# Optimization experiments

Hardware: AMD Instinct MI355X
Metric: run time of the kernel (lower is better)

## Reference

```python
import jax, jax.numpy as jnp
import numpy as np

MAX_FPS = 30.0
NUM_HEADS = 8


def _rope(x, times):
    # x: [B, H, T, D] with D even; interleaved rotary (even/odd pairs)
    B, H, T, D = x.shape
    inv_freq = 1.0 / (10000.0 ** (jnp.arange(0, D, 2, dtype=jnp.float32) / D))  # [D/2]
    pos = jnp.round(times * MAX_FPS)                       # [B, T]
    freqs = pos[:, :, None] * inv_freq[None, None, :]      # [B, T, D/2]
    cos = jnp.cos(freqs)[:, None, :, :]                    # [B, 1, T, D/2]
    sin = jnp.sin(freqs)[:, None, :, :]
    xp = x.reshape(B, H, T, D // 2, 2)
    x0, x1 = xp[..., 0], xp[..., 1]                        # even-index, odd-index elems
    r0 = x0 * cos - x1 * sin
    r1 = x0 * sin + x1 * cos
    return jnp.stack([r0, r1], axis=-1).reshape(B, H, T, D)


def setup_inputs() -> dict:
    key = jax.random.key(0)
    k1, k2, k3, k4, k5 = jax.random.split(key, 5)
    B, N, C = 4, 2048, 512
    x = jax.random.normal(k1, (B, N, C), dtype=jnp.float32)
    mask = jnp.zeros((B, N), dtype=jnp.float32)  # additive mask, 0 = attend
    # times in seconds; rounded to frame indices inside RoPE
    times = jax.random.uniform(k2, (B, N), dtype=jnp.float32) * (N / MAX_FPS)
    bound_qkv = float(np.sqrt(6.0 / (C + 3 * C)))
    Wqkv = jax.random.uniform(k3, (3 * C, C), minval=-bound_qkv, maxval=bound_qkv, dtype=jnp.float32)
    bound_p = float(np.sqrt(6.0 / (C + C)))
    Wproj = jax.random.uniform(k4, (C, C), minval=-bound_p, maxval=bound_p, dtype=jnp.float32)
    bproj = jnp.zeros((C,), dtype=jnp.float32)
    return {"x": x, "mask": mask, "times": times, "Wqkv": Wqkv,
            "Wproj": Wproj, "bproj": bproj, "num_cls_token": 0}


def reference(x, mask, times, Wqkv, Wproj, bproj, num_cls_token):
    B, N, C = x.shape
    H = NUM_HEADS
    Dh = C // H
    qkv = (x @ Wqkv.T).reshape(B, N, 3, H, Dh).transpose(2, 0, 3, 1, 4)  # [3,B,H,N,Dh]
    q, k, v = qkv[0], qkv[1], qkv[2]
    if num_cls_token > 0:
        c_q, q = q[:, :, :num_cls_token], q[:, :, num_cls_token:]
        c_k, k = k[:, :, :num_cls_token], k[:, :, num_cls_token:]
        t = times
        q = _rope(q, t)
        k = _rope(k, t)
        q = jnp.concatenate([c_q, q], axis=2)
        k = jnp.concatenate([c_k, k], axis=2)
    else:
        q = _rope(q, times)
        k = _rope(k, times)
    scale = 1.0 / jnp.sqrt(jnp.float32(Dh))
    scores = jnp.einsum('bhqd,bhkd->bhqk', q, k) * scale + mask[:, None, None, :]
    attn = jax.nn.softmax(scores, axis=-1)
    out = jnp.einsum('bhqk,bhkd->bhqd', attn, v)           # [B,H,N,Dh]
    out = out.transpose(0, 2, 1, 3).reshape(B, N, C)
    return out @ Wproj.T + bproj
```

## Files before the change

### kernel.cpp

```cpp
#include <hip/hip_runtime.h>
#include <math.h>

#define BB 4
#define NN 2048
#define CC 512
#define HH 8
#define DH 64
#define MM (BB*NN)
#define QKV_N (3*CC)
#define NSP 2

typedef _Float16 f16;
typedef __attribute__((ext_vector_type(2))) _Float16 f16x2;
typedef __attribute__((ext_vector_type(4))) _Float16 f16x4;
typedef __attribute__((ext_vector_type(8))) _Float16 f16x8;
typedef __attribute__((ext_vector_type(4))) float f32x4;
typedef __attribute__((ext_vector_type(2))) __fp16 h16x2;

#define L2E 1.4426950408889634f

#define GL16(g, l) __builtin_amdgcn_global_load_lds(                       \
    (const __attribute__((address_space(1))) void*)(g),                    \
    (__attribute__((address_space(3))) void*)(l), 16, 0, 0)

#define SX4 (MM*CC/4)
#define SW4 (QKV_N*CC/4)
#define SP4 (CC*CC/4)
__global__ __launch_bounds__(256) void cast_kernel(
    const float* __restrict__ x, const float* __restrict__ wqkv,
    const float* __restrict__ wproj,
    f16* __restrict__ xh, f16* __restrict__ wqh, f16* __restrict__ wph)
{
    const int t = blockIdx.x * 256 + threadIdx.x;
    const float* src; f16* dst; int i;
    if (t < SX4)            { src = x;     dst = xh;  i = t; }
    else if (t < SX4 + SW4) { src = wqkv;  dst = wqh; i = t - SX4; }
    else                    { src = wproj; dst = wph; i = t - SX4 - SW4; }
    f32x4 v = *(const f32x4*)(src + 4 * (size_t)i);
    f16x4 h = { (f16)v[0], (f16)v[1], (f16)v[2], (f16)v[3] };
    *(f16x4*)(dst + 4 * (size_t)i) = h;
}

__global__ __launch_bounds__(256) void rope_tab_kernel(
    const float* __restrict__ times, float2* __restrict__ tab)
{
    const int idx = blockIdx.x * 256 + threadIdx.x;
    const int row = idx >> 5, fi = idx & 31;
    const float pos = rintf(times[row] * 30.0f);
    const float invf = exp2f((float)fi * (-13.287712379549449f / 32.0f));
    float s, c;
    sincosf(pos * invf, &s, &c);
    tab[idx] = make_float2(c, s);
}

__global__ __launch_bounds__(256) void qkv_gemm(
    const f16* __restrict__ xh, const f16* __restrict__ wh,
    const float2* __restrict__ tab, const int* __restrict__ nclsp,
    f16* __restrict__ qo, f16* __restrict__ ksw, f16* __restrict__ vsw)
{
    __shared__ __align__(16) char smem[16896];
    f16 (*As)[32] = (f16 (*)[32])smem;
    f16 (*Bs)[32] = (f16 (*)[32])(smem + 8192);

    const int m0 = blockIdx.x * 128;
    const int n0 = blockIdx.y * 128;
    const int tid = threadIdx.x;
    const int lane = tid & 63;
    const int w = tid >> 6;
    const int wm = (w & 1) * 64, wn = (w >> 1) * 64;
    const int l15 = lane & 15, quad = lane >> 4;

    const int sr = tid >> 2;
    const int sc = (tid & 3) * 8;
    const f16* ga0 = xh + (size_t)(m0 + sr) * CC + sc;
    const f16* ga1 = xh + (size_t)(m0 + sr + 64) * CC + sc;
    const f16* gb0 = wh + (size_t)(n0 + sr) * CC + sc;
    const f16* gb1 = wh + (size_t)(n0 + sr + 64) * CC + sc;
    f16* la0 = &As[sr][sc];      f16* la1 = &As[sr + 64][sc];
    f16* lb0 = &Bs[sr][sc];      f16* lb1 = &Bs[sr + 64][sc];

    f32x4 acc[4][4] = {};
    for (int k0 = 0; k0 < CC; k0 += 32) {
        __syncthreads();
        GL16(ga0 + k0, la0);
        GL16(ga1 + k0, la1);
        GL16(gb0 + k0, lb0);
        GL16(gb1 + k0, lb1);
        __syncthreads();

        f16x8 af[4], bf[4];
        #pragma unroll
        for (int mi = 0; mi < 4; ++mi)
            af[mi] = *(const f16x8*)&As[wm + mi*16 + l15][quad * 8];
        #pragma unroll
        for (int ni = 0; ni < 4; ++ni)
            bf[ni] = *(const f16x8*)&Bs[wn + ni*16 + l15][quad * 8];
        #pragma unroll
        for (int mi = 0; mi < 4; ++mi)
            #pragma unroll
            for (int ni = 0; ni < 4; ++ni)
                acc[mi][ni] = __builtin_amdgcn_mfma_f32_16x16x32_f16(
                    af[mi], bf[ni], acc[mi][ni], 0, 0, 0);
    }
    __syncthreads();

    const int which = n0 >> 9;
    const int b     = m0 >> 11;
    const int mloc  = m0 & (NN - 1);
    const int hbase = (n0 & 511) >> 6;

    if (which < 2) {
        f16 (*Tr)[132] = (f16 (*)[132])smem;
        const int ncls = *nclsp;
        #pragma unroll
        for (int c = 0; c < 2; ++c) {
            if ((w & 1) == c) {
                #pragma unroll
                for (int mi = 0; mi < 4; ++mi)
                    #pragma unroll
                    for (int ni = 0; ni < 4; ++ni)
                        #pragma unroll
                        for (int r = 0; r < 4; ++r)
                            Tr[16*mi + quad*4 + r][wn + 16*ni + l15] =
                                (f16)acc[mi][ni][r];
            }
            __syncthreads();
            const int row = tid >> 2, cg = tid & 3;
            const int n   = mloc + c*64 + row;
            const int hh  = hbase + (cg >> 1);
            const int d0  = (cg & 1) * 32;
            f16x8 vv[4];
            #pragma unroll
            for (int j = 0; j < 4; ++j)
                vv[j] = *(const f16x8*)&Tr[row][cg*32 + j*8];
            if (n >= ncls) {
                const f32x4* t4 = (const f32x4*)(tab + ((size_t)b*NN + n)*32
                                                 + (d0 >> 1));
                #pragma unroll
                for (int j = 0; j < 4; ++j) {
                    f32x4 cs0 = t4[2*j];
                    f32x4 cs1 = t4[2*j + 1];
                    #pragma unroll
                    for (int p = 0; p < 4; ++p) {
                        const float co = (p < 2) ? cs0[(p & 1)*2]
                                                 : cs1[(p & 1)*2];
                        const float s  = (p < 2) ? cs0[(p & 1)*2 + 1]
                                                 : cs1[(p & 1)*2 + 1];
                        const float x0 = (float)vv[j][2*p];
                        const float x1 = (float)vv[j][2*p+1];
                        vv[j][2*p]   = (f16)(x0*co - x1*s);
                        vv[j][2*p+1] = (f16)(x0*s + x1*co);
                    }
                }
            }
            if (which == 0) {
                f16* qp = qo + (((size_t)(b*HH + hh))*NN + n)*DH + d0;
                #pragma unroll
                for (int j = 0; j < 4; ++j)
                    *(f16x8*)(qp + 8*j) = vv[j];
            } else {
                const int ktile = (mloc >> 6) + c;
                f16* kp = ksw + ((((size_t)(b*HH + hh))*32 + ktile)*64 + row)*64;
                #pragma unroll
                for (int j = 0; j < 4; ++j) {
                    const int blk = (d0 >> 3) + j;
                    *(f16x8*)(kp + ((blk ^ (row & 7)) * 8)) = vv[j];
                }
            }
            if (c == 0) __syncthreads();
        }
        return;
    }

    f16 (*Tv)[66] = (f16 (*)[66])smem;
    #pragma unroll
    for (int c = 0; c < 2; ++c) {
        if ((w & 1) == c) {
            #pragma unroll
            for (int mi = 0; mi < 4; ++mi)
                #pragma unroll
                for (int ni = 0; ni < 4; ++ni) {
                    f16x4 pk = { (f16)acc[mi][ni][0], (f16)acc[mi][ni][1],
                                 (f16)acc[mi][ni][2], (f16)acc[mi][ni][3] };
                    *(f16x4*)&Tv[wn + 16*ni + l15][16*mi + quad*4] = pk;
                }
        }
        __syncthreads();
        const int rr = tid >> 1;
        const int d  = rr & 63, hh = hbase + (rr >> 6);
        const int ktile = (mloc >> 6) + c;
        f16* vp = vsw + ((((size_t)(b*HH + hh))*32 + ktile)*64 + d)*64;
        #pragma unroll
        for (int j = 0; j < 4; ++j) {
            const int blk = (tid & 1)*4 + j;
            f16x8 t = *(const f16x8*)&Tv[rr][(tid & 1)*32 + j*8];
            *(f16x8*)(vp + ((blk ^ (d & 7)) * 8)) = t;
        }
        if (c == 0) __syncthreads();
    }
}

__global__ __launch_bounds__(256, 4) void attn_kernel(
    const f16* __restrict__ qg, const f16* __restrict__ ksw,
    const f16* __restrict__ vsw, const float* __restrict__ mask,
    f16* __restrict__ On, float* __restrict__ lbuf)
{
    __shared__ __align__(16) f16 asm_[4][4096];

    const int bh = blockIdx.x, qt = blockIdx.y, sp = blockIdx.z;
    const int b = bh >> 3, h = bh & 7;
    const int tid = threadIdx.x;
    const int w = tid >> 6, lane = tid & 63;
    const int l15 = lane & 15, quad = lane >> 4;
    const int rho = l15 & 7;

    const f16* qbase = qg + ((size_t)bh * NN + qt*128 + w*32) * DH;
    const f16* kt0 = ksw + ((size_t)bh * 32 + sp*16) * 4096;
    const f16* vt0 = vsw + ((size_t)bh * 32 + sp*16) * 4096;
    const float* mbase = mask + (size_t)b * NN + sp*1024;

    f16x8 Bq[2][2];
    #pragma unroll
    for (int ni = 0; ni < 2; ++ni)
        #pragma unroll
        for (int kc = 0; kc < 2; ++kc)
            Bq[ni][kc] = *(const f16x8*)(qbase + (size_t)(16*ni + l15) * DH
                                         + kc*32 + quad*8);

    const f16x4 Aones = (l15 == 0) ? f16x4{1.0f16, 1.0f16, 1.0f16, 1.0f16}
                                   : f16x4{0.0f16, 0.0f16, 0.0f16, 0.0f16};

    f32x4 O[2][4] = {};
    f32x4 Lacc[2] = {};
    const float scl = 0.125f * L2E;

    {
        const f16* ks = kt0 + tid*8;
        const f16* vs = vt0 + tid*8;
        GL16(ks,        &asm_[0][tid*8]);
        GL16(ks + 2048, &asm_[0][2048 + tid*8]);
        GL16(vs,        &asm_[1][tid*8]);
        GL16(vs + 2048, &asm_[1][2048 + tid*8]);
    }

    for (int kt = 0; kt < 16; ++kt) {
        const int cur = (kt & 1) * 2;
        __syncthreads();
        if (kt + 1 < 16) {
            const int nxt = 2 - cur;
            const f16* ks = kt0 + (size_t)(kt+1)*4096 + tid*8;
            const f16* vs = vt0 + (size_t)(kt+1)*4096 + tid*8;
            GL16(ks,        &asm_[nxt][tid*8]);
            GL16(ks + 2048, &asm_[nxt][2048 + tid*8]);
            GL16(vs,        &asm_[nxt+1][tid*8]);
            GL16(vs + 2048, &asm_[nxt+1][2048 + tid*8]);
        }
        const f16 (*Kh)[64] = (const f16 (*)[64])asm_[cur];
        const f16 (*Vt)[64] = (const f16 (*)[64])asm_[cur + 1];

        f32x4 mskv[4];
        #pragma unroll
        for (int mi = 0; mi < 4; ++mi) {
            f32x4 mv = *(const f32x4*)(mbase + kt*64 + 16*mi + quad*4);
            mskv[mi] = mv * L2E;
        }

        f32x4 st[4][2] = {};
        const int aw = (quad ^ rho) * 8;
        #pragma unroll
        for (int mi = 0; mi < 4; ++mi) {
            f16x8 Ak0 = *(const f16x8*)&Kh[16*mi + l15][aw];
            f16x8 Ak1 = *(const f16x8*)&Kh[16*mi + l15][aw ^ 32];
            #pragma unroll
            for (int ni = 0; ni < 2; ++ni) {
                st[mi][ni] = __builtin_amdgcn_mfma_f32_16x16x32_f16(Ak0, Bq[ni][0], st[mi][ni], 0, 0, 0);
                st[mi][ni] = __builtin_amdgcn_mfma_f32_16x16x32_f16(Ak1, Bq[ni][1], st[mi][ni], 0, 0, 0);
            }
        }

        f16x4 ph[4][2];
        #pragma unroll
        for (int ni = 0; ni < 2; ++ni)
            #pragma unroll
            for (int mi = 0; mi < 4; ++mi) {
                float e0 = exp2f(st[mi][ni][0] * scl + mskv[mi][0]);
                float e1 = exp2f(st[mi][ni][1] * scl + mskv[mi][1]);
                float e2 = exp2f(st[mi][ni][2] * scl + mskv[mi][2]);
                float e3 = exp2f(st[mi][ni][3] * scl + mskv[mi][3]);
                h16x2 lo = __builtin_amdgcn_cvt_pkrtz(e0, e1);
                h16x2 hi = __builtin_amdgcn_cvt_pkrtz(e2, e3);
                f16x2 lo2 = __builtin_bit_cast(f16x2, lo);
                f16x2 hi2 = __builtin_bit_cast(f16x2, hi);
                ph[mi][ni] = __builtin_shufflevector(lo2, hi2, 0, 1, 2, 3);
            }

        #pragma unroll
        for (int mi = 0; mi < 4; ++mi) {
            Lacc[0] = __builtin_amdgcn_mfma_f32_16x16x16f16(Aones, ph[mi][0], Lacc[0], 0, 0, 0);
            Lacc[1] = __builtin_amdgcn_mfma_f32_16x16x16f16(Aones, ph[mi][1], Lacc[1], 0, 0, 0);
            #pragma unroll
            for (int nd = 0; nd < 4; ++nd) {
                const int vb = ((2*mi + (quad >> 1)) ^ rho) * 8 + (quad & 1) * 4;
                f16x4 Av = *(const f16x4*)&Vt[16*nd + l15][vb];
                O[0][nd] = __builtin_amdgcn_mfma_f32_16x16x16f16(Av, ph[mi][0], O[0][nd], 0, 0, 0);
                O[1][nd] = __builtin_amdgcn_mfma_f32_16x16x16f16(Av, ph[mi][1], O[1][nd], 0, 0, 0);
            }
        }
    }

    #pragma unroll
    for (int ni = 0; ni < 2; ++ni) {
        const float l = __shfl(Lacc[ni][0], l15);
        const float inv = 1.0f / l;
        const int qrow = qt*128 + w*32 + 16*ni + l15;
        const size_t rbase = (size_t)sp * (32*NN) + (size_t)bh * NN + qrow;
        f16* obase = On + rbase * DH;
        #pragma unroll
        for (int nd = 0; nd < 4; ++nd) {
            f32x4 o = O[ni][nd] * inv;
            f16x4 oh = { (f16)o[0], (f16)o[1], (f16)o[2], (f16)o[3] };
            *(f16x4*)(obase + 16*nd + quad*4) = oh;
        }
        if (quad == 0)
            lbuf[rbase] = l;
    }
}

__global__ __launch_bounds__(256) void attn_merge(
    const f16* __restrict__ On, const float* __restrict__ lbuf,
    f16* __restrict__ ao)
{
    const int idx = blockIdx.x * 256 + threadIdx.x;
    const int row = idx >> 1;
    const int d0  = (idx & 1) * 32;
    const int bh = row >> 11, qrow = row & (NN - 1);
    const int b = bh >> 3, h = bh & 7;
    float ls[NSP], lt = 0.0f;
    #pragma unroll
    for (int s = 0; s < NSP; ++s) {
        ls[s] = lbuf[(size_t)s * (32*NN) + row];
        lt += ls[s];
    }
    const float inv = 1.0f / lt;
    f16* po = ao + ((size_t)b * NN + qrow) * CC + h * DH + d0;
    #pragma unroll
    for (int j = 0; j < 4; ++j) {
        float acc8[8] = {};
        #pragma unroll
        for (int s = 0; s < NSP; ++s) {
            const float ws = ls[s] * inv;
            f16x8 a = *(const f16x8*)(On + ((size_t)s*(32*NN) + row)*DH + d0 + 8*j);
            #pragma unroll
            for (int r = 0; r < 8; ++r)
                acc8[r] += ws * (float)a[r];
        }
        f16x8 o;
        #pragma unroll
        for (int r = 0; r < 8; ++r) o[r] = (f16)acc8[r];
        *(f16x8*)(po + 8*j) = o;
    }
}

__global__ __launch_bounds__(256) void proj_gemm(
    const f16* __restrict__ ah, const f16* __restrict__ wh,
    const float* __restrict__ bias, float* __restrict__ out)
{
    __shared__ f16 As[128][32];
    __shared__ f16 Bs[64][32];
    const int m0 = blockIdx.x * 128;
    const int n0 = blockIdx.y * 64;
    const int tid = threadIdx.x;
    const int lane = tid & 63;
    const int w = tid >> 6;
    const int wm = (w & 1) * 64, wn = (w >> 1) * 32;
    const int l15 = lane & 15, quad = lane >> 4;

    const int sr = tid >> 2;
    const int sc = (tid & 3) * 8;
    const f16* ga0 = ah + (size_t)(m0 + sr) * CC + sc;
    const f16* ga1 = ah + (size_t)(m0 + sr + 64) * CC + sc;
    const f16* gb0 = wh + (size_t)(n0 + sr) * CC + sc;
    f16* la0 = &As[sr][sc];      f16* la1 = &As[sr + 64][sc];
    f16* lb0 = &Bs[sr][sc];

    f32x4 acc[4][2] = {};
    for (int k0 = 0; k0 < CC; k0 += 32) {
        __syncthreads();
        GL16(ga0 + k0, la0);
        GL16(ga1 + k0, la1);
        GL16(gb0 + k0, lb0);
        __syncthreads();

        f16x8 af[4], bf[2];
        #pragma unroll
        for (int mi = 0; mi < 4; ++mi)
            af[mi] = *(const f16x8*)&As[wm + mi*16 + l15][quad * 8];
        #pragma unroll
        for (int ni = 0; ni < 2; ++ni)
            bf[ni] = *(const f16x8*)&Bs[wn + ni*16 + l15][quad * 8];
        #pragma unroll
        for (int mi = 0; mi < 4; ++mi)
            #pragma unroll
            for (int ni = 0; ni < 2; ++ni)
                acc[mi][ni] = __builtin_amdgcn_mfma_f32_16x16x32_f16(
                    af[mi], bf[ni], acc[mi][ni], 0, 0, 0);
    }

    float bb[2];
    #pragma unroll
    for (int ni = 0; ni < 2; ++ni)
        bb[ni] = bias[n0 + wn + ni*16 + l15];

    #pragma unroll
    for (int mi = 0; mi < 4; ++mi)
        #pragma unroll
        for (int r = 0; r < 4; ++r) {
            const int m = m0 + wm + mi*16 + quad*4 + r;
            #pragma unroll
            for (int ni = 0; ni < 2; ++ni)
                out[(size_t)m * CC + n0 + wn + ni*16 + l15] = acc[mi][ni][r] + bb[ni];
        }
}

extern "C" void kernel_launch(void* const* d_in, const int* in_sizes, int n_in,
                              void* d_out, int out_size, void* d_ws, size_t ws_size,
                              hipStream_t stream)
{
    const float* x     = (const float*)d_in[0];
    const float* mask  = (const float*)d_in[1];
    const float* times = (const float*)d_in[2];
    const float* Wqkv  = (const float*)d_in[3];
    const float* Wproj = (const float*)d_in[4];
    const float* bproj = (const float*)d_in[5];
    const int*   ncls  = (const int*)d_in[6];
    float* out = (float*)d_out;

    const size_t per = (size_t)BB * HH * NN * DH;
    f16* xh  = (f16*)d_ws;
    f16* wqh = xh + per;
    f16* wph = wqh + (size_t)QKV_N * CC;
    f16* q   = wph + (size_t)CC * CC;
    f16* ks  = q + per;
    f16* vs  = ks + per;
    f16* ao  = vs + per;
    f16* On  = ao + per;
    float* lb = (float*)(On + NSP * per);
    float2* tab = (float2*)(lb + NSP * 32 * NN);

    cast_kernel<<<(SX4 + SW4 + SP4) / 256, 256, 0, stream>>>(
        x, Wqkv, Wproj, xh, wqh, wph);
    rope_tab_kernel<<<(MM * 32) / 256, 256, 0, stream>>>(
        times, tab);
    qkv_gemm<<<dim3(MM / 128, QKV_N / 128), 256, 0, stream>>>(
        xh, wqh, tab, ncls, q, ks, vs);
    attn_kernel<<<dim3(BB * HH, NN / 128, NSP), 256, 0, stream>>>(
        q, ks, vs, mask, On, lb);
    attn_merge<<<(2 * 32 * NN) / 256, 256, 0, stream>>>(
        On, lb, ao);
    proj_gemm<<<dim3(MM / 128, CC / 64), 256, 0, stream>>>(
        ao, wph, bproj, out);
}
```

Baseline: 193.0 us.

## Fuse split-KV merge into projection GEMM and merge cast with rope table

The separate attn_merge kernel is removed. proj_gemm now reads both split-KV partial outputs and their row sums, combines them with weights in registers, and writes the merged tile to LDS instead of loading a precomputed attention output with async global-to-LDS loads. The cast and rope-table kernels are also merged into one launch. This removes two launches and the intermediate ao buffer round trip, but the projection A-operand load becomes a synchronous register path with extra reads that are repeated across the eight N-blocks.

```diff
diff --git a/kernel.cpp b/kernel.cpp
--- a/kernel.cpp
+++ b/kernel.cpp
@@ -9,6 +9,7 @@
 #define MM (BB*NN)
 #define QKV_N (3*CC)
 #define NSP 2
+#define SLICE ((size_t)32 * NN)
 
 typedef _Float16 f16;
 typedef __attribute__((ext_vector_type(2))) _Float16 f16x2;
@@ -26,31 +27,32 @@
 #define SX4 (MM*CC/4)
 #define SW4 (QKV_N*CC/4)
 #define SP4 (CC*CC/4)
-__global__ __launch_bounds__(256) void cast_kernel(
+#define CAST_T (SX4 + SW4 + SP4)
+#define TAB_T (MM * 32)
+__global__ __launch_bounds__(256) void cast_tab_kernel(
     const float* __restrict__ x, const float* __restrict__ wqkv,
-    const float* __restrict__ wproj,
-    f16* __restrict__ xh, f16* __restrict__ wqh, f16* __restrict__ wph)
+    const float* __restrict__ wproj, const float* __restrict__ times,
+    f16* __restrict__ xh, f16* __restrict__ wqh, f16* __restrict__ wph,
+    float2* __restrict__ tab)
 {
     const int t = blockIdx.x * 256 + threadIdx.x;
-    const float* src; f16* dst; int i;
-    if (t < SX4)            { src = x;     dst = xh;  i = t; }
-    else if (t < SX4 + SW4) { src = wqkv;  dst = wqh; i = t - SX4; }
-    else                    { src = wproj; dst = wph; i = t - SX4 - SW4; }
-    f32x4 v = *(const f32x4*)(src + 4 * (size_t)i);
-    f16x4 h = { (f16)v[0], (f16)v[1], (f16)v[2], (f16)v[3] };
-    *(f16x4*)(dst + 4 * (size_t)i) = h;
-}
-
-__global__ __launch_bounds__(256) void rope_tab_kernel(
-    const float* __restrict__ times, float2* __restrict__ tab)
-{
-    const int idx = blockIdx.x * 256 + threadIdx.x;
-    const int row = idx >> 5, fi = idx & 31;
-    const float pos = rintf(times[row] * 30.0f);
-    const float invf = exp2f((float)fi * (-13.287712379549449f / 32.0f));
-    float s, c;
-    sincosf(pos * invf, &s, &c);
-    tab[idx] = make_float2(c, s);
+    if (t < CAST_T) {
+        const float* src; f16* dst; int i;
+        if (t < SX4)            { src = x;     dst = xh;  i = t; }
+        else if (t < SX4 + SW4) { src = wqkv;  dst = wqh; i = t - SX4; }
+        else                    { src = wproj; dst = wph; i = t - SX4 - SW4; }
+        f32x4 v = *(const f32x4*)(src + 4 * (size_t)i);
+        f16x4 h = { (f16)v[0], (f16)v[1], (f16)v[2], (f16)v[3] };
+        *(f16x4*)(dst + 4 * (size_t)i) = h;
+    } else {
+        const int idx = t - CAST_T;
+        const int row = idx >> 5, fi = idx & 31;
+        const float pos = rintf(times[row] * 30.0f);
+        const float invf = exp2f((float)fi * (-13.287712379549449f / 32.0f));
+        float s, c;
+        sincosf(pos * invf, &s, &c);
+        tab[idx] = make_float2(c, s);
+    }
 }
 
 __global__ __launch_bounds__(256) void qkv_gemm(
@@ -313,7 +315,7 @@
         const float l = __shfl(Lacc[ni][0], l15);
         const float inv = 1.0f / l;
         const int qrow = qt*128 + w*32 + 16*ni + l15;
-        const size_t rbase = (size_t)sp * (32*NN) + (size_t)bh * NN + qrow;
+        const size_t rbase = (size_t)sp * SLICE + (size_t)bh * NN + qrow;
         f16* obase = On + rbase * DH;
         #pragma unroll
         for (int nd = 0; nd < 4; ++nd) {
@@ -326,44 +328,10 @@
     }
 }
 
-__global__ __launch_bounds__(256) void attn_merge(
+__global__ __launch_bounds__(256) void proj_gemm(
     const f16* __restrict__ On, const float* __restrict__ lbuf,
-    f16* __restrict__ ao)
-{
-    const int idx = blockIdx.x * 256 + threadIdx.x;
-    const int row = idx >> 1;
-    const int d0  = (idx & 1) * 32;
-    const int bh = row >> 11, qrow = row & (NN - 1);
-    const int b = bh >> 3, h = bh & 7;
-    float ls[NSP], lt = 0.0f;
-    #pragma unroll
-    for (int s = 0; s < NSP; ++s) {
-        ls[s] = lbuf[(size_t)s * (32*NN) + row];
-        lt += ls[s];
-    }
-    const float inv = 1.0f / lt;
-    f16* po = ao + ((size_t)b * NN + qrow) * CC + h * DH + d0;
-    #pragma unroll
-    for (int j = 0; j < 4; ++j) {
-        float acc8[8] = {};
-        #pragma unroll
-        for (int s = 0; s < NSP; ++s) {
-            const float ws = ls[s] * inv;
-            f16x8 a = *(const f16x8*)(On + ((size_t)s*(32*NN) + row)*DH + d0 + 8*j);
-            #pragma unroll
-            for (int r = 0; r < 8; ++r)
-                acc8[r] += ws * (float)a[r];
-        }
-        f16x8 o;
-        #pragma unroll
-        for (int r = 0; r < 8; ++r) o[r] = (f16)acc8[r];
-        *(f16x8*)(po + 8*j) = o;
-    }
-}
-
-__global__ __launch_bounds__(256) void proj_gemm(
-    const f16* __restrict__ ah, const f16* __restrict__ wh,
-    const float* __restrict__ bias, float* __restrict__ out)
+    const f16* __restrict__ wh, const float* __restrict__ bias,
+    float* __restrict__ out)
 {
     __shared__ f16 As[128][32];
     __shared__ f16 Bs[64][32];
@@ -375,20 +343,35 @@
     const int wm = (w & 1) * 64, wn = (w >> 1) * 32;
     const int l15 = lane & 15, quad = lane >> 4;
 
+    const int b  = m0 >> 11;
+    const int q0 = m0 & (NN - 1);
+
     const int sr = tid >> 2;
     const int sc = (tid & 3) * 8;
-    const f16* ga0 = ah + (size_t)(m0 + sr) * CC + sc;
-    const f16* ga1 = ah + (size_t)(m0 + sr + 64) * CC + sc;
     const f16* gb0 = wh + (size_t)(n0 + sr) * CC + sc;
-    f16* la0 = &As[sr][sc];      f16* la1 = &As[sr + 64][sc];
     f16* lb0 = &Bs[sr][sc];
 
     f32x4 acc[4][2] = {};
     for (int k0 = 0; k0 < CC; k0 += 32) {
-        __syncthreads();
-        GL16(ga0 + k0, la0);
-        GL16(ga1 + k0, la1);
+        const int h  = k0 >> 6;
+        const int d0 = k0 & 63;
+        __syncthreads();
         GL16(gb0 + k0, lb0);
+        const size_t row0 = (size_t)(b*HH + h) * NN + q0 + sr;
+        #pragma unroll
+        for (int rr = 0; rr < 2; ++rr) {
+            const size_t row = row0 + rr*64;
+            const float l0 = lbuf[row], l1 = lbuf[SLICE + row];
+            const float inv = 1.0f / (l0 + l1);
+            const float w0 = l0 * inv, w1 = l1 * inv;
+            f16x8 a0 = *(const f16x8*)(On + row * DH + d0 + sc);
+            f16x8 a1 = *(const f16x8*)(On + (SLICE + row) * DH + d0 + sc);
+            f16x8 o;
+            #pragma unroll
+            for (int r = 0; r < 8; ++r)
+                o[r] = (f16)(w0 * (float)a0[r] + w1 * (float)a1[r]);
+            *(f16x8*)&As[sr + rr*64][sc] = o;
+        }
         __syncthreads();
 
         f16x8 af[4], bf[2];
@@ -442,21 +425,16 @@
     f16* q   = wph + (size_t)CC * CC;
     f16* ks  = q + per;
     f16* vs  = ks + per;
-    f16* ao  = vs + per;
-    f16* On  = ao + per;
+    f16* On  = vs + per;
     float* lb = (float*)(On + NSP * per);
     float2* tab = (float2*)(lb + NSP * 32 * NN);
 
-    cast_kernel<<<(SX4 + SW4 + SP4) / 256, 256, 0, stream>>>(
-        x, Wqkv, Wproj, xh, wqh, wph);
-    rope_tab_kernel<<<(MM * 32) / 256, 256, 0, stream>>>(
-        times, tab);
+    cast_tab_kernel<<<(CAST_T + TAB_T) / 256, 256, 0, stream>>>(
+        x, Wqkv, Wproj, times, xh, wqh, wph, tab);
     qkv_gemm<<<dim3(MM / 128, QKV_N / 128), 256, 0, stream>>>(
         xh, wqh, tab, ncls, q, ks, vs);
     attn_kernel<<<dim3(BB * HH, NN / 128, NSP), 256, 0, stream>>>(
         q, ks, vs, mask, On, lb);
-    attn_merge<<<(2 * 32 * NN) / 256, 256, 0, stream>>>(
-        On, lb, ao);
     proj_gemm<<<dim3(MM / 128, CC / 64), 256, 0, stream>>>(
-        ao, wph, bproj, out);
+        On, lb, wph, bproj, out);
 }
```

New measurement: 191.8 us. About the same (-0.6%).
